# Kernel optimization log

Measured on AMD Instinct MI355X. Metric: run time of the kernel, lower is better.

The kernel has to match this reference:

```python
import jax, jax.numpy as jnp
import numpy as np

B, S, D = 2, 2048, 2048
H = 16
Q_LORA, KV_LORA = 1536, 512
D_NOPE, D_ROPE = 128, 64
D_QK = D_NOPE + D_ROPE  # 192
D_V = 128
EPS = 1e-6
SCALE = D_QK ** -0.5


def rms_norm(x, w):
    var = jnp.mean(jnp.square(x), axis=-1, keepdims=True)
    return x * jax.lax.rsqrt(var + EPS) * w


def apply_rotary_emb(x, freqs_cis):
    # x: [B, S, h, dr]; freqs_cis: [S, dr//2, 2] (cos, sin); interleaved pairs
    b, s, h, dr = x.shape
    xp = x.reshape(b, s, h, dr // 2, 2)
    x0, x1 = xp[..., 0], xp[..., 1]
    cos = freqs_cis[None, :, None, :, 0]
    sin = freqs_cis[None, :, None, :, 1]
    o0 = x0 * cos - x1 * sin
    o1 = x0 * sin + x1 * cos
    return jnp.stack([o0, o1], axis=-1).reshape(b, s, h, dr)


def setup_inputs() -> dict:
    key = jax.random.key(0)
    ks = jax.random.split(key, 8)
    std = 0.02
    x = jax.random.normal(ks[0], (B, S, D), jnp.float32)
    inv_freq = 1.0 / (10000.0 ** (np.arange(0, D_ROPE, 2, dtype=np.float32) / D_ROPE))
    ang = np.outer(np.arange(S, dtype=np.float32), inv_freq)  # [S, 32]
    freqs_cis = jnp.asarray(np.stack([np.cos(ang), np.sin(ang)], axis=-1))
    return {
        'x': x,
        'freqs_cis': freqs_cis,
        'Wqa': jax.random.normal(ks[1], (Q_LORA, D), jnp.float32) * std,
        'q_a_ln_w': jnp.ones((Q_LORA,), jnp.float32),
        'Wqb': jax.random.normal(ks[2], (H * D_QK, Q_LORA), jnp.float32) * std,
        'Wkva': jax.random.normal(ks[3], (KV_LORA + D_ROPE, D), jnp.float32) * std,
        'kv_a_ln_w': jnp.ones((KV_LORA,), jnp.float32),
        'Wkvb': jax.random.normal(ks[4], (H * (D_NOPE + D_V), KV_LORA), jnp.float32) * std,
        'Wo': jax.random.normal(ks[5], (D, H * D_V), jnp.float32) * std,
    }


def reference(x, freqs_cis, Wqa, q_a_ln_w, Wqb, Wkva, kv_a_ln_w, Wkvb, Wo):
    # Low-rank Q projection: down -> RMSNorm -> up
    q = rms_norm(jnp.einsum('bsd,rd->bsr', x, Wqa), q_a_ln_w)
    q = jnp.einsum('bsr,er->bse', q, Wqb).reshape(B, S, H, D_QK)
    q_nope, q_pe = q[..., :D_NOPE], q[..., D_NOPE:]
    q = jnp.concatenate([q_nope, apply_rotary_emb(q_pe, freqs_cis)], axis=-1)

    # Low-rank KV projection with shared (MQA) rope part
    kv = jnp.einsum('bsd,ed->bse', x, Wkva)
    kv_c, k_pe = kv[..., :KV_LORA], kv[..., KV_LORA:]
    kv_c = rms_norm(kv_c, kv_a_ln_w)
    k_pe = apply_rotary_emb(k_pe[:, :, None, :], freqs_cis)  # [B,S,1,D_ROPE]
    kv = jnp.einsum('bsr,er->bse', kv_c, Wkvb).reshape(B, S, H, D_NOPE + D_V)
    k_nope, v = kv[..., :D_NOPE], kv[..., D_NOPE:]
    k = jnp.concatenate(
        [k_nope, jnp.broadcast_to(k_pe, (B, S, H, D_ROPE))], axis=-1)

    # Causal SDPA with scale = qk_head_dim ** -0.5
    scores = jnp.einsum('bqhd,bkhd->bhqk', q, k) * SCALE
    causal = jnp.tril(jnp.ones((S, S), bool))
    scores = jnp.where(causal[None, None], scores, jnp.finfo(scores.dtype).min)
    probs = jax.nn.softmax(scores, axis=-1)
    out = jnp.einsum('bhqk,bkhd->bqhd', probs, v).reshape(B, S, H * D_V)
    return jnp.einsum('bse,de->bsd', out, Wo)
```

## Files before the change

### kernel.cpp

```cpp
#include <hip/hip_runtime.h>
#include <math.h>

#define B_ 2
#define S_ 2048
#define D_ 2048
#define H_ 16
#define QLORA 1536
#define KVLORA 512
#define DN 128
#define DR 64
#define DQK 192
#define DV 128
#define EPSF 1e-6f
#define SCALEF 0.07216878364870322f

typedef short short8 __attribute__((ext_vector_type(8)));
typedef float float4v __attribute__((ext_vector_type(4)));

__device__ __forceinline__ unsigned short f2bf(float f) {
    union { float f; unsigned u; } x; x.f = f;
    unsigned r = x.u + 0x7fffu + ((x.u >> 16) & 1u);
    return (unsigned short)(r >> 16);
}
__device__ __forceinline__ float bf2f(unsigned short u) {
    union { unsigned u; float f; } x; x.u = (unsigned)u << 16;
    return x.f;
}

#define GLD16(src, dst)                                                        \
    __builtin_amdgcn_global_load_lds(                                          \
        (const __attribute__((address_space(1))) void*)(src),                  \
        (__attribute__((address_space(3))) void*)(dst), 16, 0, 0)

__global__ __launch_bounds__(256) void conv_all(
        const float* __restrict__ s0, unsigned short* __restrict__ d0, long e0,
        const float* __restrict__ s1, unsigned short* __restrict__ d1, long e1,
        const float* __restrict__ s2, unsigned short* __restrict__ d2, long e2,
        const float* __restrict__ s3, unsigned short* __restrict__ d3, long e3,
        const float* __restrict__ s4, unsigned short* __restrict__ d4, long e4,
        const float* __restrict__ s5, unsigned short* __restrict__ d5) {
    long c = (long)blockIdx.x * 256 + threadIdx.x;
    const float* src;
    unsigned short* dst;
    if      (c < e0) { src = s0; dst = d0; }
    else if (c < e1) { src = s1; dst = d1; c -= e0; }
    else if (c < e2) { src = s2; dst = d2; c -= e1; }
    else if (c < e3) { src = s3; dst = d3; c -= e2; }
    else if (c < e4) { src = s4; dst = d4; c -= e3; }
    else             { src = s5; dst = d5; c -= e4; }
    const float* p = src + c * 8;
    float4 a = *(const float4*)(p);
    float4 b = *(const float4*)(p + 4);
    union { short8 v; unsigned short u[8]; } t;
    t.u[0] = f2bf(a.x); t.u[1] = f2bf(a.y); t.u[2] = f2bf(a.z); t.u[3] = f2bf(a.w);
    t.u[4] = f2bf(b.x); t.u[5] = f2bf(b.y); t.u[6] = f2bf(b.z); t.u[7] = f2bf(b.w);
    *(short8*)&dst[c * 8] = t.v;
}

#define GBM 128
#define GBN 128
#define GBK 64

template <typename OT>
__global__ __launch_bounds__(256) void gemm_t(const unsigned short* __restrict__ A,
                                              const unsigned short* __restrict__ W,
                                              OT* __restrict__ C,
                                              int M, int N, int K) {
    __shared__ unsigned short As[GBM * GBK];
    __shared__ unsigned short Ws[GBN * GBK];

    const int tid = threadIdx.x;
    const int w = tid >> 6, lane = tid & 63;
    const int l16 = lane & 15, quad = lane >> 4;
    const int wm = (w >> 1) * 64, wn = (w & 1) * 64;
    const int row0 = blockIdx.y * GBM, col0 = blockIdx.x * GBN;

    const int rL  = lane >> 3;
    const int c8g = (lane & 7) ^ rL;
    const int swzk[2] = { (((0 * 4) + quad) ^ (l16 & 7)) * 8,
                          (((1 * 4) + quad) ^ (l16 & 7)) * 8 };

    const float4v zf = {0.f, 0.f, 0.f, 0.f};
    float4v acc[4][4] = {{zf, zf, zf, zf}, {zf, zf, zf, zf},
                         {zf, zf, zf, zf}, {zf, zf, zf, zf}};

    for (int k0 = 0; k0 < K; k0 += GBK) {
        __syncthreads();
#pragma unroll
        for (int j = 0; j < 4; ++j) {
            const int ch = w * 4 + j;
            const int r = ch * 8 + rL;
            GLD16(&A[(size_t)(row0 + r) * K + k0 + c8g * 8], &As[ch * 512]);
            GLD16(&W[(size_t)(col0 + r) * K + k0 + c8g * 8], &Ws[ch * 512]);
        }
        __syncthreads();

#pragma unroll
        for (int kk = 0; kk < 2; ++kk) {
            const int swz = swzk[kk];
            short8 af[4], bf[4];
#pragma unroll
            for (int mi = 0; mi < 4; ++mi)
                af[mi] = *(const short8*)&As[(wm + mi * 16 + l16) * GBK + swz];
#pragma unroll
            for (int ni = 0; ni < 4; ++ni)
                bf[ni] = *(const short8*)&Ws[(wn + ni * 16 + l16) * GBK + swz];
#pragma unroll
            for (int mi = 0; mi < 4; ++mi)
#pragma unroll
                for (int ni = 0; ni < 4; ++ni)
                    acc[mi][ni] = __builtin_amdgcn_mfma_f32_16x16x32_bf16(af[mi], bf[ni], acc[mi][ni], 0, 0, 0);
        }
    }

#pragma unroll
    for (int mi = 0; mi < 4; ++mi)
#pragma unroll
        for (int ni = 0; ni < 4; ++ni)
#pragma unroll
            for (int r = 0; r < 4; ++r) {
                size_t idx = (size_t)(row0 + wm + mi * 16 + quad * 4 + r) * N + col0 + wn + ni * 16 + l16;
                if constexpr (sizeof(OT) == 2) C[idx] = f2bf(acc[mi][ni][r]);
                else                           C[idx] = acc[mi][ni][r];
            }
}

__global__ __launch_bounds__(256) void rmsnorm_b(const float* __restrict__ X,
                                                 const float* __restrict__ w,
                                                 unsigned short* __restrict__ Y,
                                                 int n, int ld) {
    __shared__ float tmp[4];
    const int row = blockIdx.x;
    const int tid = threadIdx.x;
    const float* x = X + (size_t)row * ld;

    float ss = 0.f;
    for (int c = tid; c < n; c += 256) {
        float v = x[c];
        ss = fmaf(v, v, ss);
    }
#pragma unroll
    for (int off = 32; off; off >>= 1) ss += __shfl_xor(ss, off, 64);
    if ((tid & 63) == 0) tmp[tid >> 6] = ss;
    __syncthreads();
    ss = tmp[0] + tmp[1] + tmp[2] + tmp[3];
    float r = rsqrtf(ss / (float)n + EPSF);

    for (int c = tid; c < n; c += 256)
        Y[(size_t)row * n + c] = f2bf(x[c] * r * w[c]);
}

__global__ __launch_bounds__(256) void kv_post(const float* __restrict__ KV,
                                               const float* __restrict__ w,
                                               const float* __restrict__ fc,
                                               unsigned short* __restrict__ kvcb,
                                               float* __restrict__ kpe,
                                               int ldkv) {
    __shared__ float tmp[4];
    const int row = blockIdx.x;
    const int s = row & (S_ - 1);
    const int tid = threadIdx.x;
    const float* kv = KV + (size_t)row * ldkv;

    float ss = 0.f;
#pragma unroll
    for (int c = tid; c < KVLORA; c += 256) {
        float v = kv[c];
        ss = fmaf(v, v, ss);
    }
#pragma unroll
    for (int off = 32; off; off >>= 1) ss += __shfl_xor(ss, off, 64);
    if ((tid & 63) == 0) tmp[tid >> 6] = ss;
    __syncthreads();
    ss = tmp[0] + tmp[1] + tmp[2] + tmp[3];
    float r = rsqrtf(ss / (float)KVLORA + EPSF);

#pragma unroll
    for (int c = tid; c < KVLORA; c += 256)
        kvcb[(size_t)row * KVLORA + c] = f2bf(kv[c] * r * w[c]);

    if (tid < 32) {
        int i = tid;
        float c0 = fc[(s * 32 + i) * 2 + 0];
        float s0 = fc[(s * 32 + i) * 2 + 1];
        float x0 = kv[KVLORA + 2 * i];
        float x1 = kv[KVLORA + 2 * i + 1];
        kpe[(size_t)row * DR + 2 * i]     = x0 * c0 - x1 * s0;
        kpe[(size_t)row * DR + 2 * i + 1] = x0 * s0 + x1 * c0;
    }
}

__global__ __launch_bounds__(256) void pack_k(const unsigned short* __restrict__ kvbb,
                                              const float* __restrict__ kpe,
                                              unsigned short* __restrict__ Kbf) {
    const int c = blockIdx.x * 256 + threadIdx.x;
    const int total = B_ * H_ * S_ * (DQK / 8);
    if (c >= total) return;
    const int d8 = c % (DQK / 8);
    const int hs = c / (DQK / 8);
    const int s  = hs % S_;
    const int bh = hs / S_;
    const int b  = bh / H_;
    const int h  = bh % H_;
    const int d  = d8 * 8;
    const int row = b * S_ + s;

    short8 v;
    if (d < DN) {
        v = *(const short8*)&kvbb[(size_t)row * (H_ * 256) + h * 256 + d];
    } else {
        const float* src = kpe + (size_t)row * DR + (d - DN);
        float4 a = *(const float4*)(src);
        float4 bb = *(const float4*)(src + 4);
        union { short8 v; unsigned short u[8]; } t;
        t.u[0] = f2bf(a.x);  t.u[1] = f2bf(a.y);  t.u[2] = f2bf(a.z);  t.u[3] = f2bf(a.w);
        t.u[4] = f2bf(bb.x); t.u[5] = f2bf(bb.y); t.u[6] = f2bf(bb.z); t.u[7] = f2bf(bb.w);
        v = t.v;
    }
    *(short8*)&Kbf[(size_t)c * 8] = v;
}

__global__ __launch_bounds__(256) void pack_vt(const unsigned short* __restrict__ kvbb,
                                               unsigned short* __restrict__ Vt) {
    __shared__ unsigned short T[DV][72];
    const int st = blockIdx.x;
    const int bh = blockIdx.y;
    const int b = bh >> 4, h = bh & 15;
    const int s0 = st * 64;
    const int tid = threadIdx.x;

    for (int c = tid; c < 64 * 16; c += 256) {
        int sp = c >> 4, ch = c & 15;
        short8 v = *(const short8*)&kvbb[(size_t)(b * S_ + s0 + sp) * (H_ * 256) + h * 256 + DN + ch * 8];
        union { short8 v; unsigned short u[8]; } t; t.v = v;
        int dv = ch * 8;
#pragma unroll
        for (int e = 0; e < 8; ++e) T[dv + e][sp] = t.u[e];
    }
    __syncthreads();
    for (int c = tid; c < 128 * 8; c += 256) {
        int dv = c >> 3, ch = c & 7;
        *(short8*)&Vt[((size_t)bh * DV + dv) * S_ + s0 + ch * 8] = *(short8*)&T[dv][ch * 8];
    }
}

#define QTILES 16
#define PROW 76

__global__ __launch_bounds__(512, 1) void flash_mfma(const unsigned short* __restrict__ Qb,
                                                     const float* __restrict__ fc,
                                                     const unsigned short* __restrict__ Kbf,
                                                     const unsigned short* __restrict__ Vt,
                                                     unsigned short* __restrict__ Ob) {
    __shared__ unsigned short Ks[2][64 * 192];
    __shared__ unsigned short Vs[2][128 * 64];
    __shared__ unsigned short Ps[8][16][PROW];

    const int bh = blockIdx.x;
    const int bx = blockIdx.y;
    const int b = bh >> 4, h = bh & 15;
    const int tid = threadIdx.x;
    const int w = tid >> 6, lane = tid & 63;
    const int l16 = lane & 15, quad = lane >> 4;
    const int sw = l16 & 7;

    const unsigned short* Kg = Kbf + (size_t)bh * S_ * DQK;
    const unsigned short* Vg = Vt + (size_t)bh * DV * S_;

    auto stage = [&](int kt_, int bufi) {
        const int kb_ = kt_ * 64;
#pragma unroll
        for (int i_ = 0; i_ < 3; ++i_) {
            int ch = (w * 3 + i_) * 64 + lane;
            int r_ = ch / 24, c_ = ch - r_ * 24;
            GLD16(&Kg[(size_t)(kb_ + r_) * DQK + ((c_ ^ (r_ & 7)) << 3)],
                  &Ks[bufi][(w * 3 + i_) * 512]);
        }
#pragma unroll
        for (int i_ = 0; i_ < 2; ++i_) {
            int ch = (w * 2 + i_) * 64 + lane;
            int r_ = ch >> 3, c_ = ch & 7;
            GLD16(&Vg[(size_t)r_ * S_ + kb_ + ((c_ ^ (r_ & 7)) << 3)],
                  &Vs[bufi][(w * 2 + i_) * 512]);
        }
    };

    for (int half = 0; half < 2; ++half) {
        const int qt = half ? (QTILES - 1 - bx) : bx;
        const int q0 = qt * 128;
        const int ntiles = 2 * qt + 2;
        const int wr0 = q0 + w * 16;

        stage(0, 0);

        short8 a_q[6];
        {
            const int s = wr0 + l16;
            const unsigned short* qrow = Qb + (size_t)(b * S_ + s) * (H_ * DQK) + h * DQK;
#pragma unroll
            for (int i = 0; i < 6; ++i) {
                short8 t = *(const short8*)&qrow[i * 32 + quad * 8];
                if (i >= 4) {
                    union { short8 v; unsigned short u[8]; } x; x.v = t;
#pragma unroll
                    for (int j = 0; j < 4; ++j) {
                        int ip = (i - 4) * 16 + quad * 4 + j;
                        float c0 = fc[(s * 32 + ip) * 2 + 0];
                        float s0 = fc[(s * 32 + ip) * 2 + 1];
                        float x0 = bf2f(x.u[2 * j]);
                        float x1 = bf2f(x.u[2 * j + 1]);
                        x.u[2 * j]     = f2bf(x0 * c0 - x1 * s0);
                        x.u[2 * j + 1] = f2bf(x0 * s0 + x1 * c0);
                    }
                    t = x.v;
                }
                a_q[i] = t;
            }
        }

        const float4v zf = {0.f, 0.f, 0.f, 0.f};
        float4v o_acc[8] = {zf, zf, zf, zf, zf, zf, zf, zf};
        float l_r[4] = {0.f, 0.f, 0.f, 0.f};

        int buf = 0;
        for (int kt = 0; kt < ntiles; ++kt) {
            const int kb = kt * 64;

            __builtin_amdgcn_s_barrier();
            if (kt + 1 < ntiles) {
                stage(kt + 1, buf ^ 1);
                asm volatile("s_waitcnt vmcnt(5)" ::: "memory");
            } else {
                asm volatile("s_waitcnt vmcnt(0)" ::: "memory");
            }
            __builtin_amdgcn_sched_barrier(0);
            __builtin_amdgcn_s_barrier();
            __builtin_amdgcn_sched_barrier(0);

            if (kb <= wr0 + 15) {
                const unsigned short* Kb_ = Ks[buf];
                const unsigned short* Vb_ = Vs[buf];

                float4v sc[4] = {zf, zf, zf, zf};
#pragma unroll
                for (int i = 0; i < 6; ++i) {
                    short8 bk[4];
#pragma unroll
                    for (int kg = 0; kg < 4; ++kg)
                        bk[kg] = *(const short8*)&Kb_[(kg * 16 + l16) * 192 + (((i * 4 + quad) ^ sw) << 3)];
#pragma unroll
                    for (int kg = 0; kg < 4; ++kg)
                        sc[kg] = __builtin_amdgcn_mfma_f32_16x16x32_bf16(a_q[i], bk[kg], sc[kg], 0, 0, 0);
                }

                const bool mneed = (kb + 63 > wr0);
#pragma unroll
                for (int kg = 0; kg < 4; ++kg) {
                    const int key = kb + kg * 16 + l16;
#pragma unroll
                    for (int r = 0; r < 4; ++r) {
                        float p = __expf(sc[kg][r] * SCALEF);
                        if (mneed && key > wr0 + quad * 4 + r) p = 0.f;
                        l_r[r] += p;
                        Ps[w][quad * 4 + r][kg * 16 + l16] = f2bf(p);
                    }
                }

#pragma unroll
                for (int kc = 0; kc < 2; ++kc) {
                    short8 pa = *(const short8*)&Ps[w][l16][kc * 32 + quad * 8];
#pragma unroll
                    for (int dvt = 0; dvt < 8; ++dvt) {
                        short8 vb = *(const short8*)&Vb_[(dvt * 16 + l16) * 64 + (((kc * 4 + quad) ^ sw) << 3)];
                        o_acc[dvt] = __builtin_amdgcn_mfma_f32_16x16x32_bf16(pa, vb, o_acc[dvt], 0, 0, 0);
                    }
                }
            }
            buf ^= 1;
        }

#pragma unroll
        for (int r = 0; r < 4; ++r) {
            float t = l_r[r];
            t += __shfl_xor(t, 1);
            t += __shfl_xor(t, 2);
            t += __shfl_xor(t, 4);
            t += __shfl_xor(t, 8);
            l_r[r] = t;
        }
#pragma unroll
        for (int r = 0; r < 4; ++r) {
            float inv = 1.f / l_r[r];
            int row = wr0 + quad * 4 + r;
            unsigned short* op = Ob + (size_t)(b * S_ + row) * (H_ * DV) + h * DV;
#pragma unroll
            for (int dvt = 0; dvt < 8; ++dvt)
                op[dvt * 16 + l16] = f2bf(o_acc[dvt][r] * inv);
        }
    }
}

extern "C" void kernel_launch(void* const* d_in, const int* in_sizes, int n_in,
                              void* d_out, int out_size, void* d_ws, size_t ws_size,
                              hipStream_t stream) {
    const float* x    = (const float*)d_in[0];
    const float* fc   = (const float*)d_in[1];
    const float* Wqa  = (const float*)d_in[2];
    const float* qlw  = (const float*)d_in[3];
    const float* Wqb  = (const float*)d_in[4];
    const float* Wkva = (const float*)d_in[5];
    const float* kvw  = (const float*)d_in[6];
    const float* Wkvb = (const float*)d_in[7];
    const float* Wo   = (const float*)d_in[8];
    float* out = (float*)d_out;

    const int M = B_ * S_;
    const int NQKV = QLORA + 640;
    char* wsb = (char*)d_ws;

    unsigned short* qb  = (unsigned short*)wsb;
    unsigned short* Wob = (unsigned short*)(wsb + 25165824);
    char* R2 = wsb + 50331648;
    float*          qlkv  = (float*)R2;
    unsigned short* xb    = (unsigned short*)(R2 + 35651584);
    unsigned short* Wcat  = (unsigned short*)(R2 + 52428800);
    unsigned short* kvbb  = (unsigned short*)R2;
    unsigned short* attnb = (unsigned short*)R2;
    char* R3 = R2 + 67108864;
    unsigned short* qlatb = (unsigned short*)R3;
    unsigned short* Wqbb  = (unsigned short*)(R3 + 12582912);
    unsigned short* Kbf   = (unsigned short*)R3;
    char* R4 = R3 + 25165824;
    float*          kpe   = (float*)R4;
    unsigned short* kvcb  = (unsigned short*)(R4 + 1048576);
    unsigned short* Wkvbb = (unsigned short*)(R4 + 5242880);
    unsigned short* Vt    = (unsigned short*)R4;

    {
        const long e0 = 1048576;
        const long e1 = e0 + 393216;
        const long e2 = e1 + 147456;
        const long e3 = e2 + 589824;
        const long e4 = e3 + 262144;
        const long tot = e4 + 524288;
        conv_all<<<(int)(tot / 256), 256, 0, stream>>>(
            x, xb, e0,
            Wqa, Wcat, e1,
            Wkva, Wcat + (size_t)QLORA * D_, e2,
            Wqb, Wqbb, e3,
            Wkvb, Wkvbb, e4,
            Wo, Wob);
    }

    gemm_t<float><<<dim3(NQKV / GBN, M / GBM), 256, 0, stream>>>(xb, Wcat, qlkv, M, NQKV, D_);

    rmsnorm_b<<<M, 256, 0, stream>>>(qlkv, qlw, qlatb, QLORA, NQKV);
    kv_post<<<M, 256, 0, stream>>>(qlkv + QLORA, kvw, fc, kvcb, kpe, NQKV);

    gemm_t<unsigned short><<<dim3(H_ * DQK / GBN, M / GBM), 256, 0, stream>>>(qlatb, Wqbb, qb, M, H_ * DQK, QLORA);
    gemm_t<unsigned short><<<dim3(H_ * 256 / GBN, M / GBM), 256, 0, stream>>>(kvcb, Wkvbb, kvbb, M, H_ * 256, KVLORA);

    {
        int total = B_ * H_ * S_ * (DQK / 8);
        pack_k<<<(total + 255) / 256, 256, 0, stream>>>(kvbb, kpe, Kbf);
        pack_vt<<<dim3(S_ / 64, B_ * H_), 256, 0, stream>>>(kvbb, Vt);
    }

    flash_mfma<<<dim3(B_ * H_, QTILES / 2), 512, 0, stream>>>(qb, fc, Kbf, Vt, attnb);

    gemm_t<float><<<dim3(D_ / GBN, M / GBM), 256, 0, stream>>>(attnb, Wob, out, M, D_, D_);
}
```

Before: 451.4 us.

## Fuse K packing into the KV up-projection epilogue and add MFMA priority hints

Removes the separate pack_k kernel and the fp32 kpe buffer. The KV up-projection GEMM now writes k_nope directly into the per-head K layout, and kv_post writes the bf16 rotary key part broadcast to all heads. This cuts a full read and write pass over K and one kernel launch. kv_post is moved after the Q up-projection so that its writes into the aliased workspace do not clobber Q inputs. The attention kernel also raises wave priority around its MFMA loops with s_setprio, aiming for better interleaving with softmax work.

```diff
diff --git a/kernel.cpp b/kernel.cpp
--- a/kernel.cpp
+++ b/kernel.cpp
@@ -125,6 +125,77 @@
             }
 }
 
+__global__ __launch_bounds__(256) void gemm_kv(const unsigned short* __restrict__ A,
+                                               const unsigned short* __restrict__ W,
+                                               unsigned short* __restrict__ kvbb,
+                                               unsigned short* __restrict__ Kbf,
+                                               int M, int N, int K) {
+    __shared__ unsigned short As[GBM * GBK];
+    __shared__ unsigned short Ws[GBN * GBK];
+
+    const int tid = threadIdx.x;
+    const int w = tid >> 6, lane = tid & 63;
+    const int l16 = lane & 15, quad = lane >> 4;
+    const int wm = (w >> 1) * 64, wn = (w & 1) * 64;
+    const int row0 = blockIdx.y * GBM, col0 = blockIdx.x * GBN;
+    const int h = blockIdx.x >> 1, vhalf = blockIdx.x & 1;
+
+    const int rL  = lane >> 3;
+    const int c8g = (lane & 7) ^ rL;
+    const int swzk[2] = { (((0 * 4) + quad) ^ (l16 & 7)) * 8,
+                          (((1 * 4) + quad) ^ (l16 & 7)) * 8 };
+
+    const float4v zf = {0.f, 0.f, 0.f, 0.f};
+    float4v acc[4][4] = {{zf, zf, zf, zf}, {zf, zf, zf, zf},
+                         {zf, zf, zf, zf}, {zf, zf, zf, zf}};
+
+    for (int k0 = 0; k0 < K; k0 += GBK) {
+        __syncthreads();
+#pragma unroll
+        for (int j = 0; j < 4; ++j) {
+            const int ch = w * 4 + j;
+            const int r = ch * 8 + rL;
+            GLD16(&A[(size_t)(row0 + r) * K + k0 + c8g * 8], &As[ch * 512]);
+            GLD16(&W[(size_t)(col0 + r) * K + k0 + c8g * 8], &Ws[ch * 512]);
+        }
+        __syncthreads();
+
+#pragma unroll
+        for (int kk = 0; kk < 2; ++kk) {
+            const int swz = swzk[kk];
+            short8 af[4], bf[4];
+#pragma unroll
+            for (int mi = 0; mi < 4; ++mi)
+                af[mi] = *(const short8*)&As[(wm + mi * 16 + l16) * GBK + swz];
+#pragma unroll
+            for (int ni = 0; ni < 4; ++ni)
+                bf[ni] = *(const short8*)&Ws[(wn + ni * 16 + l16) * GBK + swz];
+#pragma unroll
+            for (int mi = 0; mi < 4; ++mi)
+#pragma unroll
+                for (int ni = 0; ni < 4; ++ni)
+                    acc[mi][ni] = __builtin_amdgcn_mfma_f32_16x16x32_bf16(af[mi], bf[ni], acc[mi][ni], 0, 0, 0);
+        }
+    }
+
+#pragma unroll
+    for (int mi = 0; mi < 4; ++mi)
+#pragma unroll
+        for (int ni = 0; ni < 4; ++ni)
+#pragma unroll
+            for (int r = 0; r < 4; ++r) {
+                const int row = row0 + wm + mi * 16 + quad * 4 + r;
+                const int d = wn + ni * 16 + l16;
+                const unsigned short v = f2bf(acc[mi][ni][r]);
+                if (vhalf) {
+                    kvbb[(size_t)row * N + col0 + d] = v;
+                } else {
+                    const int b = row >> 11, s = row & (S_ - 1);
+                    Kbf[((size_t)(b * H_ + h) * S_ + s) * DQK + d] = v;
+                }
+            }
+}
+
 __global__ __launch_bounds__(256) void rmsnorm_b(const float* __restrict__ X,
                                                  const float* __restrict__ w,
                                                  unsigned short* __restrict__ Y,
@@ -154,11 +225,12 @@
                                                const float* __restrict__ w,
                                                const float* __restrict__ fc,
                                                unsigned short* __restrict__ kvcb,
-                                               float* __restrict__ kpe,
+                                               unsigned short* __restrict__ Kbf,
                                                int ldkv) {
     __shared__ float tmp[4];
     const int row = blockIdx.x;
     const int s = row & (S_ - 1);
+    const int b = row >> 11;
     const int tid = threadIdx.x;
     const float* kv = KV + (size_t)row * ldkv;
 
@@ -185,39 +257,15 @@
         float s0 = fc[(s * 32 + i) * 2 + 1];
         float x0 = kv[KVLORA + 2 * i];
         float x1 = kv[KVLORA + 2 * i + 1];
-        kpe[(size_t)row * DR + 2 * i]     = x0 * c0 - x1 * s0;
-        kpe[(size_t)row * DR + 2 * i + 1] = x0 * s0 + x1 * c0;
-    }
-}
-
-__global__ __launch_bounds__(256) void pack_k(const unsigned short* __restrict__ kvbb,
-                                              const float* __restrict__ kpe,
-                                              unsigned short* __restrict__ Kbf) {
-    const int c = blockIdx.x * 256 + threadIdx.x;
-    const int total = B_ * H_ * S_ * (DQK / 8);
-    if (c >= total) return;
-    const int d8 = c % (DQK / 8);
-    const int hs = c / (DQK / 8);
-    const int s  = hs % S_;
-    const int bh = hs / S_;
-    const int b  = bh / H_;
-    const int h  = bh % H_;
-    const int d  = d8 * 8;
-    const int row = b * S_ + s;
-
-    short8 v;
-    if (d < DN) {
-        v = *(const short8*)&kvbb[(size_t)row * (H_ * 256) + h * 256 + d];
-    } else {
-        const float* src = kpe + (size_t)row * DR + (d - DN);
-        float4 a = *(const float4*)(src);
-        float4 bb = *(const float4*)(src + 4);
-        union { short8 v; unsigned short u[8]; } t;
-        t.u[0] = f2bf(a.x);  t.u[1] = f2bf(a.y);  t.u[2] = f2bf(a.z);  t.u[3] = f2bf(a.w);
-        t.u[4] = f2bf(bb.x); t.u[5] = f2bf(bb.y); t.u[6] = f2bf(bb.z); t.u[7] = f2bf(bb.w);
-        v = t.v;
-    }
-    *(short8*)&Kbf[(size_t)c * 8] = v;
+        unsigned short b0 = f2bf(x0 * c0 - x1 * s0);
+        unsigned short b1 = f2bf(x0 * s0 + x1 * c0);
+#pragma unroll
+        for (int h = 0; h < H_; ++h) {
+            unsigned short* kp = Kbf + ((size_t)(b * H_ + h) * S_ + s) * DQK + DN;
+            kp[2 * i]     = b0;
+            kp[2 * i + 1] = b1;
+        }
+    }
 }
 
 __global__ __launch_bounds__(256) void pack_vt(const unsigned short* __restrict__ kvbb,
@@ -342,6 +390,7 @@
                 const unsigned short* Vb_ = Vs[buf];
 
                 float4v sc[4] = {zf, zf, zf, zf};
+                __builtin_amdgcn_s_setprio(1);
 #pragma unroll
                 for (int i = 0; i < 6; ++i) {
                     short8 bk[4];
@@ -352,6 +401,7 @@
                     for (int kg = 0; kg < 4; ++kg)
                         sc[kg] = __builtin_amdgcn_mfma_f32_16x16x32_bf16(a_q[i], bk[kg], sc[kg], 0, 0, 0);
                 }
+                __builtin_amdgcn_s_setprio(0);
 
                 const bool mneed = (kb + 63 > wr0);
 #pragma unroll
@@ -366,6 +416,7 @@
                     }
                 }
 
+                __builtin_amdgcn_s_setprio(1);
 #pragma unroll
                 for (int kc = 0; kc < 2; ++kc) {
                     short8 pa = *(const short8*)&Ps[w][l16][kc * 32 + quad * 8];
@@ -375,6 +426,7 @@
                         o_acc[dvt] = __builtin_amdgcn_mfma_f32_16x16x32_bf16(pa, vb, o_acc[dvt], 0, 0, 0);
                     }
                 }
+                __builtin_amdgcn_s_setprio(0);
             }
             buf ^= 1;
         }
@@ -431,7 +483,6 @@
     unsigned short* Wqbb  = (unsigned short*)(R3 + 12582912);
     unsigned short* Kbf   = (unsigned short*)R3;
     char* R4 = R3 + 25165824;
-    float*          kpe   = (float*)R4;
     unsigned short* kvcb  = (unsigned short*)(R4 + 1048576);
     unsigned short* Wkvbb = (unsigned short*)(R4 + 5242880);
     unsigned short* Vt    = (unsigned short*)R4;
@@ -455,16 +506,14 @@
     gemm_t<float><<<dim3(NQKV / GBN, M / GBM), 256, 0, stream>>>(xb, Wcat, qlkv, M, NQKV, D_);
 
     rmsnorm_b<<<M, 256, 0, stream>>>(qlkv, qlw, qlatb, QLORA, NQKV);
-    kv_post<<<M, 256, 0, stream>>>(qlkv + QLORA, kvw, fc, kvcb, kpe, NQKV);
 
     gemm_t<unsigned short><<<dim3(H_ * DQK / GBN, M / GBM), 256, 0, stream>>>(qlatb, Wqbb, qb, M, H_ * DQK, QLORA);
-    gemm_t<unsigned short><<<dim3(H_ * 256 / GBN, M / GBM), 256, 0, stream>>>(kvcb, Wkvbb, kvbb, M, H_ * 256, KVLORA);
-
-    {
-        int total = B_ * H_ * S_ * (DQK / 8);
-        pack_k<<<(total + 255) / 256, 256, 0, stream>>>(kvbb, kpe, Kbf);
-        pack_vt<<<dim3(S_ / 64, B_ * H_), 256, 0, stream>>>(kvbb, Vt);
-    }
+
+    kv_post<<<M, 256, 0, stream>>>(qlkv + QLORA, kvw, fc, kvcb, Kbf, NQKV);
+
+    gemm_kv<<<dim3(H_ * 256 / GBN, M / GBM), 256, 0, stream>>>(kvcb, Wkvbb, kvbb, Kbf, M, H_ * 256, KVLORA);
+
+    pack_vt<<<dim3(S_ / 64, B_ * H_), 256, 0, stream>>>(kvbb, Vt);
 
     flash_mfma<<<dim3(B_ * H_, QTILES / 2), 512, 0, stream>>>(qb, fc, Kbf, Vt, attnb);
 
```

Result: slower. 466.9 us (+3.4%).
